# Kernel optimization log

Hardware: AMD Instinct MI355X
Metric: run time of the kernel (lower is better)

The kernel has to match this reference:

```python
import jax, jax.numpy as jnp
import numpy as np

OOV_INDEX = 1  # stand-in for params.OOV_INDEX
H = 1024
VOCAB = 50000
L = 2048


def setup_inputs() -> dict:
    key = jax.random.key(0)
    ks = jax.random.split(key, 10)
    s = 0.05
    inp = {
        "input_ids": jax.random.randint(ks[0], (L,), 0, VOCAB),
        "embedding": jax.random.normal(ks[1], (VOCAB, H), jnp.float32) * s,
        "fwd_W_ih": jax.random.normal(ks[2], (3 * H, H), jnp.float32) * s,
        "fwd_W_hh": jax.random.normal(ks[3], (3 * H, H), jnp.float32) * s,
        "fwd_b_ih": jax.random.normal(ks[4], (3 * H,), jnp.float32) * s,
        "fwd_b_hh": jax.random.normal(ks[5], (3 * H,), jnp.float32) * s,
        "rev_W_ih": jax.random.normal(ks[6], (3 * H, H), jnp.float32) * s,
        "rev_W_hh": jax.random.normal(ks[7], (3 * H, H), jnp.float32) * s,
        "rev_b_ih": jax.random.normal(ks[8], (3 * H,), jnp.float32) * s,
        "rev_b_hh": jax.random.normal(ks[9], (3 * H,), jnp.float32) * s,
    }
    return inp


def _gru_scan(x_seq, W_ih, W_hh, b_ih, b_hh):
    # x_seq: [L, H]. PyTorch GRU gate order: r, z, n.
    gx = x_seq @ W_ih.T + b_ih  # [L, 3H], input projections precomputed

    def step(h, gx_t):
        gh = h @ W_hh.T + b_hh
        gx_r, gx_z, gx_n = jnp.split(gx_t, 3)
        gh_r, gh_z, gh_n = jnp.split(gh, 3)
        r = jax.nn.sigmoid(gx_r + gh_r)
        z = jax.nn.sigmoid(gx_z + gh_z)
        n = jnp.tanh(gx_n + r * gh_n)
        h_new = (1.0 - z) * n + z * h
        return h_new, h_new

    h0 = jnp.zeros((x_seq.shape[1],), x_seq.dtype)
    h_last, outs = jax.lax.scan(step, h0, gx)
    return outs, h_last  # [L, H], [H]


def reference(input_ids, embedding, fwd_W_ih, fwd_W_hh, fwd_b_ih, fwd_b_hh,
              rev_W_ih, rev_W_hh, rev_b_ih, rev_b_hh):
    # Embedding lookup; OOV index -> zero vector (empty_vector in original)
    embeds = embedding[input_ids]  # [L, H]
    embeds = jnp.where((input_ids == OOV_INDEX)[:, None], 0.0, embeds)

    fwd_outputs, fwd_h = _gru_scan(embeds, fwd_W_ih, fwd_W_hh, fwd_b_ih, fwd_b_hh)
    rev_outs_rev, rev_h = _gru_scan(embeds[::-1], rev_W_ih, rev_W_hh, rev_b_ih, rev_b_hh)
    rev_outputs = rev_outs_rev[::-1]  # place back at original positions

    outputs = jnp.concatenate([fwd_outputs, rev_outputs], axis=1)  # [L, 2H]
    hidden = jnp.concatenate([fwd_h, rev_h])[None, None, :]        # [1, 1, 2H]
    projected_output = hidden
    return outputs, hidden, projected_output
```

## Files before the change

### kernel.cpp

```cpp
#include <hip/hip_runtime.h>
#include <math.h>

#define SEQL 2048
#define H 1024
#define G3 3072
#define SENT 1.0e30f

__device__ __forceinline__ float sigmoidf_(float x){ return 1.0f/(1.0f+expf(-x)); }

__device__ __forceinline__ float4 ld_cohere(const float* p){
  float4 r;
  asm volatile("global_load_dwordx4 %0, %1, off sc0 sc1\n\t"
               "s_waitcnt vmcnt(0)"
               : "=&v"(r) : "v"(p) : "memory");
  return r;
}
__device__ __forceinline__ void st_cohere(float* p, float2 v){
  asm volatile("global_store_dwordx2 %0, %1, off sc0 sc1"
               :: "v"(p), "v"(v) : "memory");
}

__global__ __launch_bounds__(256) void init_sent(float* p, int n4){
  int i = blockIdx.x*256 + threadIdx.x;
  if (i < n4) ((float4*)p)[i] = make_float4(SENT,SENT,SENT,SENT);
}

__global__ __launch_bounds__(256) void embed_kernel(const int* __restrict__ ids,
                                                    const float* __restrict__ emb,
                                                    float* __restrict__ out){
  int t = blockIdx.x;
  int id = ids[t];
  const float4* src = (const float4*)(emb + (size_t)id*H);
  float4* dst = (float4*)(out + (size_t)t*H);
  float4 v = (id == 1) ? make_float4(0.f,0.f,0.f,0.f) : src[threadIdx.x];
  dst[threadIdx.x] = v;
}

__global__ __launch_bounds__(256) void gemm_kernel(const float* __restrict__ A,
  const float* __restrict__ WF, const float* __restrict__ WR,
  const float* __restrict__ bF, const float* __restrict__ bR,
  float* __restrict__ gxF, float* __restrict__ gxR)
{
  __shared__ float As[16][68];
  __shared__ float Bs[16][68];
  const int tid = threadIdx.x;
  const int n0 = blockIdx.x * 64;
  const int m0 = blockIdx.y * 64;
  const int dir = (n0 >= G3);
  const float* B    = dir ? WR : WF;
  const float* bias = dir ? bR : bF;
  float* C          = dir ? gxR : gxF;
  const int j0 = dir ? (n0 - G3) : n0;

  const int lr = tid >> 2;
  const int lc = (tid & 3) * 4;
  const int tx = tid & 15;
  const int ty = tid >> 4;

  float acc[4][4] = {};

  for (int k0 = 0; k0 < H; k0 += 16){
    float4 av = *(const float4*)(A + (size_t)(m0+lr)*H + k0 + lc);
    float4 bv = *(const float4*)(B + (size_t)(j0+lr)*H + k0 + lc);
    As[lc+0][lr]=av.x; As[lc+1][lr]=av.y; As[lc+2][lr]=av.z; As[lc+3][lr]=av.w;
    Bs[lc+0][lr]=bv.x; Bs[lc+1][lr]=bv.y; Bs[lc+2][lr]=bv.z; Bs[lc+3][lr]=bv.w;
    __syncthreads();
    #pragma unroll
    for (int kk=0; kk<16; ++kk){
      float a0=As[kk][ty*4+0], a1=As[kk][ty*4+1], a2=As[kk][ty*4+2], a3=As[kk][ty*4+3];
      float b0=Bs[kk][tx*4+0], b1=Bs[kk][tx*4+1], b2=Bs[kk][tx*4+2], b3=Bs[kk][tx*4+3];
      acc[0][0]=fmaf(a0,b0,acc[0][0]); acc[0][1]=fmaf(a0,b1,acc[0][1]);
      acc[0][2]=fmaf(a0,b2,acc[0][2]); acc[0][3]=fmaf(a0,b3,acc[0][3]);
      acc[1][0]=fmaf(a1,b0,acc[1][0]); acc[1][1]=fmaf(a1,b1,acc[1][1]);
      acc[1][2]=fmaf(a1,b2,acc[1][2]); acc[1][3]=fmaf(a1,b3,acc[1][3]);
      acc[2][0]=fmaf(a2,b0,acc[2][0]); acc[2][1]=fmaf(a2,b1,acc[2][1]);
      acc[2][2]=fmaf(a2,b2,acc[2][2]); acc[2][3]=fmaf(a2,b3,acc[2][3]);
      acc[3][0]=fmaf(a3,b0,acc[3][0]); acc[3][1]=fmaf(a3,b1,acc[3][1]);
      acc[3][2]=fmaf(a3,b2,acc[3][2]); acc[3][3]=fmaf(a3,b3,acc[3][3]);
    }
    __syncthreads();
  }

  #pragma unroll
  for (int u=0; u<4; ++u){
    float4 o;
    o.x = acc[u][0] + bias[j0+tx*4+0];
    o.y = acc[u][1] + bias[j0+tx*4+1];
    o.z = acc[u][2] + bias[j0+tx*4+2];
    o.w = acc[u][3] + bias[j0+tx*4+3];
    *(float4*)(C + (size_t)(m0+ty*4+u)*G3 + j0 + tx*4) = o;
  }
}

__global__ __launch_bounds__(256, 1) void scan_kernel(
  const float* __restrict__ gxF, const float* __restrict__ gxR,
  const float* __restrict__ WhF, const float* __restrict__ WhR,
  const float* __restrict__ bhF, const float* __restrict__ bhR,
  float* hFbuf, float* hRbuf, float* __restrict__ out)
{
  const int wgid = blockIdx.x;
  const int dir  = wgid >> 7;
  const int d    = wgid & 127;
  const int i0   = d * 8;
  const int tid  = threadIdx.x;
  const int lane = tid & 63;
  const int wv   = tid >> 6;

  const float* gx  = dir ? gxR : gxF;
  const float* Whh = dir ? WhR : WhF;
  const float* bhh = dir ? bhR : bhF;
  float* hbuf      = dir ? hRbuf : hFbuf;

  const int ia = i0 + 2*wv;
  const int ib = ia + 1;
  const int rows[6] = { ia, H+ia, 2*H+ia, ib, H+ib, 2*H+ib };

  float w[6][16];
  float bias[6];
  #pragma unroll
  for (int rr=0; rr<6; ++rr){
    const float* wp = Whh + (size_t)rows[rr]*H + lane;
    #pragma unroll
    for (int m=0; m<16; ++m) w[rr][m] = wp[m*64];
    bias[rr] = bhh[rows[rr]];
  }

  __shared__ float hs[H];

  for (int s=0; s<SEQL; ++s){
    const int t = dir ? (SEQL-1-s) : s;
    const float* gxt = gx + (size_t)t*G3;
    float g0 = gxt[ia],     g1 = gxt[H+ia],   g2 = gxt[2*H+ia];
    float g3 = gxt[ib],     g4 = gxt[H+ib],   g5 = gxt[2*H+ib];

    if (s == 0){
      #pragma unroll
      for (int q=0;q<4;++q) hs[tid*4+q] = 0.0f;
    } else {
      const float* src = hbuf + (size_t)(s-1)*H + tid*4;
      float4 v;
      do { v = ld_cohere(src); }
      while (v.x==SENT || v.y==SENT || v.z==SENT || v.w==SENT);
      hs[tid*4+0]=v.x; hs[tid*4+1]=v.y; hs[tid*4+2]=v.z; hs[tid*4+3]=v.w;
    }
    __syncthreads();

    float hv[16];
    #pragma unroll
    for (int m=0; m<16; ++m) hv[m] = hs[lane + 64*m];

    float dots[6];
    #pragma unroll
    for (int rr=0; rr<6; ++rr){
      float acc = 0.f;
      #pragma unroll
      for (int m=0; m<16; ++m) acc = fmaf(w[rr][m], hv[m], acc);
      #pragma unroll
      for (int off=32; off>0; off>>=1) acc += __shfl_xor(acc, off);
      dots[rr] = acc + bias[rr];
    }

    const float hpa = hs[ia], hpb = hs[ib];

    float ra = sigmoidf_(g0 + dots[0]);
    float za = sigmoidf_(g1 + dots[1]);
    float na = tanhf    (g2 + ra*dots[2]);
    float hna = (1.f - za)*na + za*hpa;

    float rb = sigmoidf_(g3 + dots[3]);
    float zb = sigmoidf_(g4 + dots[4]);
    float nb = tanhf    (g5 + rb*dots[5]);
    float hnb = (1.f - zb)*nb + zb*hpb;

    if (lane == 0){
      st_cohere(hbuf + (size_t)s*H + ia, make_float2(hna, hnb));
      *(float2*)(out + (size_t)t*2048 + dir*H + ia) = make_float2(hna, hnb);
      if (s == SEQL-1){
        const size_t base = (size_t)SEQL*2048;
        *(float2*)(out + base + dir*H + ia)        = make_float2(hna, hnb);
        *(float2*)(out + base + 2048 + dir*H + ia) = make_float2(hna, hnb);
      }
    }
    __syncthreads();
  }
}

extern "C" void kernel_launch(void* const* d_in, const int* in_sizes, int n_in,
                              void* d_out, int out_size, void* d_ws, size_t ws_size,
                              hipStream_t stream)
{
  const int*   ids  = (const int*)  d_in[0];
  const float* emb  = (const float*)d_in[1];
  const float* WihF = (const float*)d_in[2];
  const float* WhhF = (const float*)d_in[3];
  const float* bihF = (const float*)d_in[4];
  const float* bhhF = (const float*)d_in[5];
  const float* WihR = (const float*)d_in[6];
  const float* WhhR = (const float*)d_in[7];
  const float* bihR = (const float*)d_in[8];
  const float* bhhR = (const float*)d_in[9];
  float* out = (float*)d_out;
  float* ws  = (float*)d_ws;

  float* embeds = ws;
  float* gxF    = embeds + (size_t)SEQL*H;
  float* gxR    = gxF + (size_t)SEQL*G3;
  float* hF     = gxR + (size_t)SEQL*G3;
  float* hR     = hF + (size_t)SEQL*H;

  init_sent<<<4096, 256, 0, stream>>>(hF, 1048576);
  embed_kernel<<<SEQL, 256, 0, stream>>>(ids, emb, embeds);
  dim3 gg(96, 32);
  gemm_kernel<<<gg, 256, 0, stream>>>(embeds, WihF, WihR, bihF, bihR, gxF, gxR);
  scan_kernel<<<256, 256, 0, stream>>>(gxF, gxR, WhhF, WhhR, bhhF, bhhR, hF, hR, out);
}
```

Before: 6.689 ms.

## Use one hidden unit per wave with 512-thread scan workgroups

Doubles the scan workgroup to 512 threads (8 waves) so each wave computes a single hidden unit's three gate dot products instead of two units' six. This halves the per-wave serial FMA and reduction chain on each recurrent step and spreads the h broadcast load across more threads with dword2 polling. The cost is more waves contending for barriers and polling per step, plus narrower coherent stores. Empty asm constraints pin the weights in VGPRs.

```diff
diff --git a/kernel.cpp b/kernel.cpp
--- a/kernel.cpp
+++ b/kernel.cpp
@@ -8,15 +8,15 @@
 
 __device__ __forceinline__ float sigmoidf_(float x){ return 1.0f/(1.0f+expf(-x)); }
 
-__device__ __forceinline__ float4 ld_cohere(const float* p){
-  float4 r;
-  asm volatile("global_load_dwordx4 %0, %1, off sc0 sc1\n\t"
+__device__ __forceinline__ float2 ld_cohere2(const float* p){
+  float2 r;
+  asm volatile("global_load_dwordx2 %0, %1, off sc0 sc1\n\t"
                "s_waitcnt vmcnt(0)"
                : "=&v"(r) : "v"(p) : "memory");
   return r;
 }
-__device__ __forceinline__ void st_cohere(float* p, float2 v){
-  asm volatile("global_store_dwordx2 %0, %1, off sc0 sc1"
+__device__ __forceinline__ void st_cohere1(float* p, float v){
+  asm volatile("global_store_dword %0, %1, off sc0 sc1"
                :: "v"(p), "v"(v) : "memory");
 }
 
@@ -92,7 +92,7 @@
   }
 }
 
-__global__ __launch_bounds__(256, 1) void scan_kernel(
+__global__ __launch_bounds__(512, 1) void scan_kernel(
   const float* __restrict__ gxF, const float* __restrict__ gxR,
   const float* __restrict__ WhF, const float* __restrict__ WhR,
   const float* __restrict__ bhF, const float* __restrict__ bhR,
@@ -111,18 +111,23 @@
   const float* bhh = dir ? bhR : bhF;
   float* hbuf      = dir ? hRbuf : hFbuf;
 
-  const int ia = i0 + 2*wv;
-  const int ib = ia + 1;
-  const int rows[6] = { ia, H+ia, 2*H+ia, ib, H+ib, 2*H+ib };
-
-  float w[6][16];
-  float bias[6];
+  const int ia = i0 + wv;
+  const int rows[3] = { ia, H+ia, 2*H+ia };
+
+  float w[3][16];
+  float bias[3];
   #pragma unroll
-  for (int rr=0; rr<6; ++rr){
+  for (int rr=0; rr<3; ++rr){
     const float* wp = Whh + (size_t)rows[rr]*H + lane;
     #pragma unroll
     for (int m=0; m<16; ++m) w[rr][m] = wp[m*64];
     bias[rr] = bhh[rows[rr]];
+  }
+  #pragma unroll
+  for (int rr=0; rr<3; ++rr){
+    #pragma unroll
+    for (int m=0; m<16; ++m) asm volatile("" : "+v"(w[rr][m]));
+    asm volatile("" : "+v"(bias[rr]));
   }
 
   __shared__ float hs[H];
@@ -130,18 +135,16 @@
   for (int s=0; s<SEQL; ++s){
     const int t = dir ? (SEQL-1-s) : s;
     const float* gxt = gx + (size_t)t*G3;
-    float g0 = gxt[ia],     g1 = gxt[H+ia],   g2 = gxt[2*H+ia];
-    float g3 = gxt[ib],     g4 = gxt[H+ib],   g5 = gxt[2*H+ib];
+    float g0 = gxt[ia], g1 = gxt[H+ia], g2 = gxt[2*H+ia];
 
     if (s == 0){
-      #pragma unroll
-      for (int q=0;q<4;++q) hs[tid*4+q] = 0.0f;
+      hs[tid*2+0] = 0.0f; hs[tid*2+1] = 0.0f;
     } else {
-      const float* src = hbuf + (size_t)(s-1)*H + tid*4;
-      float4 v;
-      do { v = ld_cohere(src); }
-      while (v.x==SENT || v.y==SENT || v.z==SENT || v.w==SENT);
-      hs[tid*4+0]=v.x; hs[tid*4+1]=v.y; hs[tid*4+2]=v.z; hs[tid*4+3]=v.w;
+      const float* src = hbuf + (size_t)(s-1)*H + tid*2;
+      float2 v;
+      do { v = ld_cohere2(src); }
+      while (v.x==SENT || v.y==SENT);
+      hs[tid*2+0]=v.x; hs[tid*2+1]=v.y;
     }
     __syncthreads();
 
@@ -149,9 +152,9 @@
     #pragma unroll
     for (int m=0; m<16; ++m) hv[m] = hs[lane + 64*m];
 
-    float dots[6];
-    #pragma unroll
-    for (int rr=0; rr<6; ++rr){
+    float dots[3];
+    #pragma unroll
+    for (int rr=0; rr<3; ++rr){
       float acc = 0.f;
       #pragma unroll
       for (int m=0; m<16; ++m) acc = fmaf(w[rr][m], hv[m], acc);
@@ -160,25 +163,19 @@
       dots[rr] = acc + bias[rr];
     }
 
-    const float hpa = hs[ia], hpb = hs[ib];
-
-    float ra = sigmoidf_(g0 + dots[0]);
-    float za = sigmoidf_(g1 + dots[1]);
-    float na = tanhf    (g2 + ra*dots[2]);
-    float hna = (1.f - za)*na + za*hpa;
-
-    float rb = sigmoidf_(g3 + dots[3]);
-    float zb = sigmoidf_(g4 + dots[4]);
-    float nb = tanhf    (g5 + rb*dots[5]);
-    float hnb = (1.f - zb)*nb + zb*hpb;
+    const float hp = hs[ia];
+    float r = sigmoidf_(g0 + dots[0]);
+    float z = sigmoidf_(g1 + dots[1]);
+    float n = tanhf    (g2 + r*dots[2]);
+    float hn = (1.f - z)*n + z*hp;
 
     if (lane == 0){
-      st_cohere(hbuf + (size_t)s*H + ia, make_float2(hna, hnb));
-      *(float2*)(out + (size_t)t*2048 + dir*H + ia) = make_float2(hna, hnb);
+      st_cohere1(hbuf + (size_t)s*H + ia, hn);
+      out[(size_t)t*2048 + dir*H + ia] = hn;
       if (s == SEQL-1){
         const size_t base = (size_t)SEQL*2048;
-        *(float2*)(out + base + dir*H + ia)        = make_float2(hna, hnb);
-        *(float2*)(out + base + 2048 + dir*H + ia) = make_float2(hna, hnb);
+        out[base + dir*H + ia]        = hn;
+        out[base + 2048 + dir*H + ia] = hn;
       }
     }
     __syncthreads();
@@ -212,5 +209,5 @@
   embed_kernel<<<SEQL, 256, 0, stream>>>(ids, emb, embeds);
   dim3 gg(96, 32);
   gemm_kernel<<<gg, 256, 0, stream>>>(embeds, WihF, WihR, bihF, bihR, gxF, gxR);
-  scan_kernel<<<256, 256, 0, stream>>>(gxF, gxR, WhhF, WhhR, bhhF, bhhR, hF, hR, out);
-}
+  scan_kernel<<<256, 512, 0, stream>>>(gxF, gxR, WhhF, WhhR, bhhF, bhhR, hF, hR, out);
+}
```

Result: faster. 6.236 ms (-6.8%).

## Pack recurrent weights as fp16 in AGPRs and use fdot2 in scan

Applied to the files above, without the earlier changes.

Each workgroup of the GRU scan kernel now has 512 threads and owns 16 hidden units. The launch uses 512 blocks, and six of every eight exit immediately, presumably so the survivors spread across different XCDs/CUs. Recurrent weights are converted to packed fp16 and kept in accumulator registers. The dot products use v_dot2 on fp16 pairs with fp32 accumulation. The polled hidden state uses L2-scoped loads, with an occasional uncached load, and is double-buffered in shared memory so the trailing barrier can go. The reduced-precision weights and hidden state add rounding error over 2048 recurrent steps, and the changed coherence scope risks stale reads.

```diff
diff --git a/kernel.cpp b/kernel.cpp
--- a/kernel.cpp
+++ b/kernel.cpp
@@ -6,16 +6,38 @@
 #define G3 3072
 #define SENT 1.0e30f
 
+typedef __fp16   fp16x2  __attribute__((ext_vector_type(2)));
+typedef _Float16 half2_t __attribute__((ext_vector_type(2)));
+
 __device__ __forceinline__ float sigmoidf_(float x){ return 1.0f/(1.0f+expf(-x)); }
 
-__device__ __forceinline__ float4 ld_cohere(const float* p){
+__device__ __forceinline__ uint32_t pk_u(float a, float b){
+  fp16x2 h = __builtin_amdgcn_cvt_pkrtz(a, b);
+  union{fp16x2 h; uint32_t u;} c; c.h = h; return c.u;
+}
+__device__ __forceinline__ half2_t u_as_h2(uint32_t x){
+  union{half2_t h; uint32_t u;} c; c.u = x; return c.h;
+}
+
+__device__ __forceinline__ float4 ld_l2(const float* p){
+  float4 r;
+  asm volatile("global_load_dwordx4 %0, %1, off sc0\n\t"
+               "s_waitcnt vmcnt(0)"
+               : "=&v"(r) : "v"(p) : "memory");
+  return r;
+}
+__device__ __forceinline__ float4 ld_uc(const float* p){
   float4 r;
   asm volatile("global_load_dwordx4 %0, %1, off sc0 sc1\n\t"
                "s_waitcnt vmcnt(0)"
                : "=&v"(r) : "v"(p) : "memory");
   return r;
 }
-__device__ __forceinline__ void st_cohere(float* p, float2 v){
+__device__ __forceinline__ void st_l2_2(float* p, float2 v){
+  asm volatile("global_store_dwordx2 %0, %1, off sc0"
+               :: "v"(p), "v"(v) : "memory");
+}
+__device__ __forceinline__ void st_uc_2(float* p, float2 v){
   asm volatile("global_store_dwordx2 %0, %1, off sc0 sc1"
                :: "v"(p), "v"(v) : "memory");
 }
@@ -92,16 +114,18 @@
   }
 }
 
-__global__ __launch_bounds__(256, 1) void scan_kernel(
+__global__ __launch_bounds__(512, 4) void scan_kernel(
   const float* __restrict__ gxF, const float* __restrict__ gxR,
   const float* __restrict__ WhF, const float* __restrict__ WhR,
   const float* __restrict__ bhF, const float* __restrict__ bhR,
   float* hFbuf, float* hRbuf, float* __restrict__ out)
 {
-  const int wgid = blockIdx.x;
-  const int dir  = wgid >> 7;
-  const int d    = wgid & 127;
-  const int i0   = d * 8;
+  const int bid  = blockIdx.x;
+  const int role = bid & 7;
+  if (role >= 2) return;
+  const int dir  = role;
+  const int rank = bid >> 3;
+  const int i0   = rank * 16;
   const int tid  = threadIdx.x;
   const int lane = tid & 63;
   const int wv   = tid >> 6;
@@ -115,52 +139,85 @@
   const int ib = ia + 1;
   const int rows[6] = { ia, H+ia, 2*H+ia, ib, H+ib, 2*H+ib };
 
-  float w[6][16];
-  float bias[6];
+  uint32_t wa[48];
+  float    ba[6];
   #pragma unroll
   for (int rr=0; rr<6; ++rr){
-    const float* wp = Whh + (size_t)rows[rr]*H + lane;
-    #pragma unroll
-    for (int m=0; m<16; ++m) w[rr][m] = wp[m*64];
-    bias[rr] = bhh[rows[rr]];
-  }
-
-  __shared__ float hs[H];
+    const float* wp = Whh + (size_t)rows[rr]*H;
+    #pragma unroll
+    for (int q=0; q<4; ++q){
+      float4 w4 = *(const float4*)(wp + q*256 + lane*4);
+      uint32_t u0 = pk_u(w4.x, w4.y);
+      uint32_t u1 = pk_u(w4.z, w4.w);
+      asm volatile("v_accvgpr_write_b32 %0, %1" : "=a"(wa[rr*8+q*2+0]) : "v"(u0));
+      asm volatile("v_accvgpr_write_b32 %0, %1" : "=a"(wa[rr*8+q*2+1]) : "v"(u1));
+    }
+    float bb = bhh[rows[rr]];
+    asm volatile("v_accvgpr_write_b32 %0, %1" : "=a"(ba[rr]) : "v"(bb));
+  }
+
+  __shared__ float    hs_f[2][H];
+  __shared__ uint32_t hs_p[2][H/2];
 
   for (int s=0; s<SEQL; ++s){
+    const int b = s & 1;
     const int t = dir ? (SEQL-1-s) : s;
     const float* gxt = gx + (size_t)t*G3;
-    float g0 = gxt[ia],     g1 = gxt[H+ia],   g2 = gxt[2*H+ia];
-    float g3 = gxt[ib],     g4 = gxt[H+ib],   g5 = gxt[2*H+ib];
-
-    if (s == 0){
-      #pragma unroll
-      for (int q=0;q<4;++q) hs[tid*4+q] = 0.0f;
-    } else {
-      const float* src = hbuf + (size_t)(s-1)*H + tid*4;
+    float g0 = gxt[ia], g1 = gxt[H+ia], g2 = gxt[2*H+ia];
+    float g3 = gxt[ib], g4 = gxt[H+ib], g5 = gxt[2*H+ib];
+
+    if (tid < 256){
       float4 v;
-      do { v = ld_cohere(src); }
-      while (v.x==SENT || v.y==SENT || v.z==SENT || v.w==SENT);
-      hs[tid*4+0]=v.x; hs[tid*4+1]=v.y; hs[tid*4+2]=v.z; hs[tid*4+3]=v.w;
+      if (s == 0){
+        v = make_float4(0.f,0.f,0.f,0.f);
+      } else {
+        const float* src = hbuf + (size_t)(s-1)*H + tid*4;
+        int it = 0;
+        for (;;){
+          v = ((++it & 3) != 0) ? ld_l2(src) : ld_uc(src);
+          if (!(v.x==SENT || v.y==SENT || v.z==SENT || v.w==SENT)) break;
+        }
+      }
+      *(float4*)&hs_f[b][tid*4] = v;
+      uint2 pk;
+      pk.x = pk_u(v.x, v.y);
+      pk.y = pk_u(v.z, v.w);
+      *(uint2*)&hs_p[b][tid*2] = pk;
     }
     __syncthreads();
 
-    float hv[16];
-    #pragma unroll
-    for (int m=0; m<16; ++m) hv[m] = hs[lane + 64*m];
+    uint32_t hp[8];
+    #pragma unroll
+    for (int q=0; q<4; ++q){
+      uint2 u = *(const uint2*)&hs_p[b][q*128 + lane*2];
+      hp[q*2+0] = u.x; hp[q*2+1] = u.y;
+    }
 
     float dots[6];
     #pragma unroll
     for (int rr=0; rr<6; ++rr){
       float acc = 0.f;
       #pragma unroll
-      for (int m=0; m<16; ++m) acc = fmaf(w[rr][m], hv[m], acc);
+      for (int tt=0; tt<8; ++tt){
+        uint32_t wu;
+        asm volatile("v_accvgpr_read_b32 %0, %1" : "=v"(wu) : "a"(wa[rr*8+tt]));
+        acc = __builtin_amdgcn_fdot2(u_as_h2(wu), u_as_h2(hp[tt]), acc, false);
+      }
+      dots[rr] = acc;
+    }
+    #pragma unroll
+    for (int off=32; off>0; off>>=1){
       #pragma unroll
-      for (int off=32; off>0; off>>=1) acc += __shfl_xor(acc, off);
-      dots[rr] = acc + bias[rr];
-    }
-
-    const float hpa = hs[ia], hpb = hs[ib];
+      for (int rr=0; rr<6; ++rr) dots[rr] += __shfl_xor(dots[rr], off);
+    }
+    #pragma unroll
+    for (int rr=0; rr<6; ++rr){
+      float bv;
+      asm volatile("v_accvgpr_read_b32 %0, %1" : "=v"(bv) : "a"(ba[rr]));
+      dots[rr] += bv;
+    }
+
+    const float hpa = hs_f[b][ia], hpb = hs_f[b][ib];
 
     float ra = sigmoidf_(g0 + dots[0]);
     float za = sigmoidf_(g1 + dots[1]);
@@ -173,15 +230,17 @@
     float hnb = (1.f - zb)*nb + zb*hpb;
 
     if (lane == 0){
-      st_cohere(hbuf + (size_t)s*H + ia, make_float2(hna, hnb));
-      *(float2*)(out + (size_t)t*2048 + dir*H + ia) = make_float2(hna, hnb);
+      float2 h2v = make_float2(hna, hnb);
+      float* dst = hbuf + (size_t)s*H + ia;
+      st_l2_2(dst, h2v);
+      st_uc_2(dst, h2v);
+      *(float2*)(out + (size_t)t*2048 + dir*H + ia) = h2v;
       if (s == SEQL-1){
         const size_t base = (size_t)SEQL*2048;
-        *(float2*)(out + base + dir*H + ia)        = make_float2(hna, hnb);
-        *(float2*)(out + base + 2048 + dir*H + ia) = make_float2(hna, hnb);
+        *(float2*)(out + base + dir*H + ia)        = h2v;
+        *(float2*)(out + base + 2048 + dir*H + ia) = h2v;
       }
     }
-    __syncthreads();
   }
 }
 
@@ -212,5 +271,5 @@
   embed_kernel<<<SEQL, 256, 0, stream>>>(ids, emb, embeds);
   dim3 gg(96, 32);
   gemm_kernel<<<gg, 256, 0, stream>>>(embeds, WihF, WihR, bihF, bihR, gxF, gxR);
-  scan_kernel<<<256, 256, 0, stream>>>(gxF, gxR, WhhF, WhhR, bhhF, bhhR, hF, hR, out);
-}
+  scan_kernel<<<512, 512, 0, stream>>>(gxF, gxR, WhhF, WhhR, bhhF, bhhR, hF, hR, out);
+}
```

Result: slower. 16.90 ms (+152.6%).
